# Performance work log

Hardware: AMD Instinct MI355X
Metric: run time of the kernel (lower is better)

Reference implementation:

```python
import jax, jax.numpy as jnp
import numpy as np

INPUT_DIM = 256
OUTPUT_DIM = 16
MAX_HIDDEN = 768
NUM_NODES = INPUT_DIM + OUTPUT_DIM + MAX_HIDDEN          # 1040
NUM_MIDDLE = OUTPUT_DIM + MAX_HIDDEN                     # 784
BATCH = 32768


def setup_inputs() -> dict:
    key = jax.random.key(0)
    k1, k2, k3, k4 = jax.random.split(key, 4)
    x = jax.random.normal(k1, (BATCH, INPUT_DIM), dtype=jnp.float32)
    weight = jax.random.normal(k2, (NUM_NODES, NUM_MIDDLE), dtype=jnp.float32) * 0.1
    bias = jax.random.normal(k3, (NUM_MIDDLE,), dtype=jnp.float32) * 0.1
    connectivity = jax.random.randint(k4, (NUM_NODES, NUM_MIDDLE), 0, 2, dtype=jnp.int32)
    node_existence = jnp.ones((NUM_MIDDLE,), dtype=jnp.int32)
    return {
        "x": x,
        "weight": weight,
        "bias": bias,
        "connectivity": connectivity,
        "node_existence": node_existence,
        "output_dim": OUTPUT_DIM,
    }


def reference(x, weight, bias, connectivity, node_existence, output_dim):
    B = x.shape[0]
    N, M = weight.shape                 # num_nodes, num_middle_result_nodes
    input_dim = N - M
    eff = weight * connectivity.astype(weight.dtype)   # [N, M] masked weights
    ex = node_existence.astype(weight.dtype)           # [M]
    results0 = jnp.zeros((B, N), dtype=x.dtype).at[:, :input_dim].set(x)
    node_idx = jnp.arange(N)

    def step(results, i):
        # only nodes < input_dim + i feed node i (faithful to growing slice)
        valid = (node_idx < input_dim + i).astype(eff.dtype)   # [N]
        w_col = jnp.take(eff, i, axis=1) * valid               # [N]
        res = results @ w_col                                   # [B]
        res = (jax.nn.sigmoid(res) + bias[i]) * ex[i]
        results = jax.lax.dynamic_update_slice(results, res[:, None], (0, input_dim + i))
        return results, None

    results, _ = jax.lax.scan(step, results0, jnp.arange(M))
    return results[:, -output_dim:]
```

## Files before the change

kernel.cpp:

```cpp
#include <hip/hip_runtime.h>
#include <cstdint>
#include <cstddef>

#define INPUT_DIM 256
#define OUT_DIM   16
#define NMID      784
#define NNODE     1040
#define MROW      768
#define KB        16
#define NBLK      49
#define NMCH      24
#define BATCH     32768
#define UNITW     520
#define XROW      264

typedef float f32x4 __attribute__((ext_vector_type(4)));
typedef __bf16 bf16x8 __attribute__((ext_vector_type(8)));

#define GLL16(gp, lp)                                                        \
  __builtin_amdgcn_global_load_lds(                                          \
      (const __attribute__((address_space(1))) unsigned int*)(gp),           \
      (__attribute__((address_space(3))) unsigned int*)(lp), 16, 0, 0)

static __device__ __forceinline__ unsigned int f2bf(float f) {
  unsigned int u = __builtin_bit_cast(unsigned int, f);
  u += 0x7fffu + ((u >> 16) & 1u);
  return u >> 16;
}
static __device__ __forceinline__ float bf2f(unsigned short h) {
  unsigned int u = ((unsigned int)h) << 16;
  return __builtin_bit_cast(float, u);
}
static __device__ __forceinline__ float bflo(unsigned int w) {
  return __builtin_bit_cast(float, w << 16);
}
static __device__ __forceinline__ float bfhi(unsigned int w) {
  return __builtin_bit_cast(float, w & 0xffff0000u);
}

__global__ __launch_bounds__(256) void prep_efft(
    const float* __restrict__ w, const int* __restrict__ conn,
    const int* __restrict__ ex, unsigned short* __restrict__ effX,
    unsigned short* __restrict__ effM) {
  __shared__ unsigned short tile[64][66];
  const int j0 = blockIdx.x * 64;
  const int i0 = blockIdx.y * 64;
  const int tx = threadIdx.x & 63;
  const int ty = threadIdx.x >> 6;
  const int i  = i0 + tx;
  for (int t = 0; t < 16; ++t) {
    int j = j0 + t * 4 + ty;
    float v = 0.f;
    if (j < NNODE && i < NMID && j < INPUT_DIM + i) {
      float e = (j >= INPUT_DIM) ? (float)ex[j - INPUT_DIM] : 1.f;
      v = w[(size_t)j * NMID + i] * (float)conn[(size_t)j * NMID + i] * e;
    }
    tile[t * 4 + ty][tx] = (unsigned short)f2bf(v);
  }
  __syncthreads();
  const int i_loc = threadIdx.x >> 2;
  const int jq    = threadIdx.x & 3;
  const int iw    = i0 + i_loc;
  const int jbase = j0 + jq * 16;
  if (iw < NMID) {
    if (jbase + 16 <= INPUT_DIM) {
      #pragma unroll
      for (int c = 0; c < 16; ++c)
        effX[(size_t)iw * INPUT_DIM + jbase + c] = tile[jq * 16 + c][i_loc];
    } else if (jbase >= INPUT_DIM && (jbase - INPUT_DIM + 16) <= MROW) {
      #pragma unroll
      for (int c = 0; c < 16; ++c)
        effM[(size_t)iw * MROW + (jbase - INPUT_DIM) + c] =
            tile[jq * 16 + c][i_loc];
    }
  }
}

__global__ __launch_bounds__(64) void prep_cvec(
    const unsigned short* __restrict__ effM, const float* __restrict__ w,
    const int* __restrict__ conn, const int* __restrict__ ex,
    const float* __restrict__ bias, float* __restrict__ cvec) {
  const int i = blockIdx.x;
  const int l = threadIdx.x;
  float s = 0.f;
  for (int jm = l; jm < MROW; jm += 64)
    s += bf2f(effM[(size_t)i * MROW + jm]) * bias[jm];
  {
    int jm = MROW + l;
    if (jm < NMID && jm < i) {
      size_t idx = (size_t)(INPUT_DIM + jm) * NMID + i;
      s += w[idx] * (float)conn[idx] * (float)ex[jm] * bias[jm];
    }
  }
  for (int off = 32; off; off >>= 1) s += __shfl_down(s, off, 64);
  if (l == 0) cvec[i] = s;
}

__global__ __launch_bounds__(256) void prep_wpack(
    const float* __restrict__ w, const int* __restrict__ conn,
    const int* __restrict__ ex, const float* __restrict__ cvec,
    unsigned short* __restrict__ wpk) {
  const int b = blockIdx.x;
  const int k = threadIdx.x >> 4;
  const int c = threadIdx.x & 15;
  const int src = KB * b + k;
  const int dst = KB * b + c;
  float v = 0.f;
  if (k < c) {
    size_t idx = (size_t)(INPUT_DIM + src) * NMID + dst;
    v = w[idx] * (float)conn[idx] * (float)ex[src];
  } else if (k == c) {
    v = cvec[src];
  }
  wpk[b * 256 + k * 16 + c] = (unsigned short)f2bf(v);
}

__global__ __launch_bounds__(256)
__attribute__((amdgpu_waves_per_eu(2, 4))) void pgemm(
    const float* __restrict__ x, const unsigned short* __restrict__ effX,
    unsigned short* __restrict__ Pt, int slab_off, int slabsz) {
  __shared__ __align__(16) unsigned short xs[64][XROW];

  const int tid = threadIdx.x;
  const int l   = tid & 63;
  const int wv  = tid >> 6;
  const int g   = l >> 4;
  const int r16 = l & 15;
  const int bb  = blockIdx.x * 64;

  {
    const int row = tid >> 2;
    const int q   = tid & 3;
    const float* xr = x + (size_t)(slab_off + bb + row) * INPUT_DIM + q * 64;
    unsigned short* xd = &xs[row][q * 64];
    #pragma unroll
    for (int i = 0; i < 16; ++i) {
      float4 v = *(const float4*)(xr + 4 * i);
      uint2 u;
      u.x = f2bf(v.x) | (f2bf(v.y) << 16);
      u.y = f2bf(v.z) | (f2bf(v.w) << 16);
      *(uint2*)(xd + 4 * i) = u;
    }
  }
  __syncthreads();

  for (int nb = wv; nb < NBLK; nb += 4) {
    const unsigned short* ap =
        effX + (size_t)(nb * 16 + r16) * INPUT_DIM + 8 * g;
    uint4 a[8];
    #pragma unroll
    for (int c = 0; c < 8; ++c) a[c] = *(const uint4*)(ap + 32 * c);

    #pragma unroll
    for (int s = 0; s < 4; ++s) {
      f32x4 acc = {0.f, 0.f, 0.f, 0.f};
      #pragma unroll
      for (int c = 0; c < 8; ++c) {
        uint4 braw = *(const uint4*)&xs[s * 16 + r16][32 * c + 8 * g];
        acc = __builtin_amdgcn_mfma_f32_16x16x32_bf16(
            __builtin_bit_cast(bf16x8, a[c]), __builtin_bit_cast(bf16x8, braw),
            acc, 0, 0, 0);
      }
      #pragma unroll
      for (int i = 0; i < 4; ++i)
        Pt[(size_t)(nb * 16 + 4 * g + i) * slabsz + bb + s * 16 + r16] =
            (unsigned short)f2bf(acc[i]);
    }
  }
}

__global__ __launch_bounds__(256)
__attribute__((amdgpu_waves_per_eu(2, 2))) void net_main(
    const unsigned short* __restrict__ Pt,
    const unsigned short* __restrict__ effM,
    const unsigned short* __restrict__ wpk,
    const float* __restrict__ bias, const int* __restrict__ ex,
    float* __restrict__ out, int slab_off, int slabsz) {
  __shared__ __align__(16) unsigned short Bs[2][3][8][UNITW];
  __shared__ __align__(16) unsigned short wtriL[2][256];
  __shared__ float scrS[4][320];

  const int tid = threadIdx.x;
  const int l   = tid & 63;
  const int wv  = tid >> 6;
  const int g   = l >> 4;
  const int r16 = l & 15;
  const int rb  = (blockIdx.x * 4 + wv) * 16;
  float* myscr = scrS[wv];

  uint4 sfrag[NMCH];
  #pragma unroll
  for (int c = 0; c < NMCH; ++c) {
    uint4 z; z.x = z.y = z.z = z.w = 0u;
    sfrag[c] = z;
  }

#define STAGE_B(nb, t)                                                        \
  {                                                                           \
    _Pragma("unroll")                                                         \
    for (int q_ = 0; q_ < 2; ++q_) {                                          \
      const int rp_ = wv + 4 * q_;                             \
      const int r_  = 2 * rp_ + (l >> 5);                    \
      const int cl_ = (l & 31) ^ (r_ & 7);                                    \
      const unsigned short* gs_ =                                             \
          effM + (size_t)(16 * (t) + r_) * MROW + cl_ * 8;                    \
      GLL16(gs_, &Bs[nb][0][rp_][0]);                                         \
      if ((t) >= 17) GLL16(gs_ + 256, &Bs[nb][1][rp_][0]);                    \
      if ((t) >= 33) GLL16(gs_ + 512, &Bs[nb][2][rp_][0]);                    \
    }                                                                         \
  }

  if (wv == 0) {
    uint2 t0 = *(const uint2*)(wpk + l * 4);
    *(uint2*)&wtriL[0][l * 4] = t0;
  }
  __syncthreads();

  for (int b = 0; b < NBLK; ++b) {
    const int cur = b & 1;

    if (b + 1 < NBLK) {
      STAGE_B(cur ^ 1, b + 1);
      if (wv == 0) {
        uint2 tw = *(const uint2*)(wpk + (b + 1) * 256 + l * 4);
        *(uint2*)&wtriL[cur ^ 1][l * 4] = tw;
      }
    }

    uint2 praw = *(const uint2*)(Pt + (size_t)(KB * b + r16) * slabsz +
                                 rb + 4 * g);

    f32x4 ac0 = {0.f, 0.f, 0.f, 0.f}, ac1 = ac0, ac2 = ac0, ac3 = ac0;
#define CHUNK(c)                                                              \
  {                                                                           \
    const int pp_ = (c) >> 3, cc_ = (c) & 7;                                  \
    uint4 braw = *(const uint4*)&Bs[cur][pp_][r16 >> 1]                       \
        [(r16 & 1) * 256 + (((cc_ * 4 + g) ^ (r16 & 7)) * 8)];                \
    f32x4& a_ = ((c) & 3) == 0 ? ac0 : ((c) & 3) == 1 ? ac1                   \
               : ((c) & 3) == 2 ? ac2 : ac3;                                  \
    a_ = __builtin_amdgcn_mfma_f32_16x16x32_bf16(                             \
        __builtin_bit_cast(bf16x8, sfrag[(c)]),                               \
        __builtin_bit_cast(bf16x8, braw), a_, 0, 0, 0);                       \
  }
    if (b >= 1) {
      CHUNK(0) CHUNK(1) CHUNK(2) CHUNK(3)
      CHUNK(4) CHUNK(5) CHUNK(6) CHUNK(7)
    }
    if (b >= 17) {
      CHUNK(8) CHUNK(9) CHUNK(10) CHUNK(11)
      CHUNK(12) CHUNK(13) CHUNK(14) CHUNK(15)
    }
    if (b >= 33) {
      CHUNK(16) CHUNK(17) CHUNK(18) CHUNK(19)
      CHUNK(20) CHUNK(21) CHUNK(22) CHUNK(23)
    }
#undef CHUNK
    f32x4 accsum = (ac0 + ac1) + (ac2 + ac3);
    accsum[0] += bflo(praw.x);
    accsum[1] += bfhi(praw.x);
    accsum[2] += bflo(praw.y);
    accsum[3] += bfhi(praw.y);

    #pragma unroll
    for (int i = 0; i < 4; ++i)
      myscr[(4 * g + i) * 20 + r16] = accsum[i];
    float acc_t[16];
    #pragma unroll
    for (int c = 0; c < 16; ++c)
      acc_t[c] = myscr[r16 * 20 + c];

    const unsigned short* wt = wtriL[cur];
    #pragma unroll
    for (int k = 0; k < 16; ++k) {
      const uint4 w0 = *(const uint4*)&wt[k * 16];
      const uint4 w1 = *(const uint4*)&wt[k * 16 + 8];
      const unsigned int wd[8] = {w0.x, w0.y, w0.z, w0.w,
                                  w1.x, w1.y, w1.z, w1.w};
      float xk = acc_t[k] + ((k & 1) ? bfhi(wd[k >> 1]) : bflo(wd[k >> 1]));
      float s  = __builtin_amdgcn_rcpf(
          1.f + __builtin_amdgcn_exp2f(xk * -1.44269504088896341f));
      acc_t[k] = s;
      #pragma unroll
      for (int c = k + 1; c < 16; ++c) {
        float wc = (c & 1) ? bfhi(wd[c >> 1]) : bflo(wd[c >> 1]);
        acc_t[c] = __builtin_fmaf(s, wc, acc_t[c]);
      }
    }

    if (b == NBLK - 1) {
      const size_t orow = (size_t)(slab_off + rb + r16) * OUT_DIM;
      #pragma unroll
      for (int i = 0; i < 4; ++i) {
        int oc = 4 * g + i;
        int mi = NMID - OUT_DIM + oc;
        out[orow + oc] = (acc_t[oc] + bias[mi]) * (float)ex[mi];
      }
    } else {
      const int cml = (b >> 1) & 7;
      const int vb = 8 * (g & 1);
      uint4 packed;
      packed.x = f2bf(acc_t[vb + 0]) | (f2bf(acc_t[vb + 1]) << 16);
      packed.y = f2bf(acc_t[vb + 2]) | (f2bf(acc_t[vb + 3]) << 16);
      packed.z = f2bf(acc_t[vb + 4]) | (f2bf(acc_t[vb + 5]) << 16);
      packed.w = f2bf(acc_t[vb + 6]) | (f2bf(acc_t[vb + 7]) << 16);
      const bool part = ((g >> 1) == (b & 1));
#define PACKW(base)                                                           \
  {                                                                           \
    _Pragma("unroll")                                                         \
    for (int c2 = 0; c2 < 8; ++c2)                                            \
      if (c2 == cml) {                                                        \
        if (part) sfrag[(base) + c2] = packed;                                \
      }                                                                       \
  }
      if (b < 16) {
        PACKW(0)
      } else if (b < 32) {
        PACKW(8)
      } else {
        PACKW(16)
      }
#undef PACKW
    }

    __syncthreads();
  }
#undef STAGE_B
}

extern "C" void kernel_launch(void* const* d_in, const int* in_sizes, int n_in,
                              void* d_out, int out_size, void* d_ws, size_t ws_size,
                              hipStream_t stream) {
  const float* x      = (const float*)d_in[0];
  const float* weight = (const float*)d_in[1];
  const float* bias   = (const float*)d_in[2];
  const int*   conn   = (const int*)d_in[3];
  const int*   ex     = (const int*)d_in[4];

  char* ws = (char*)d_ws;
  size_t off = 0;
  unsigned short* effX = (unsigned short*)(ws + off); off += (size_t)NMID * INPUT_DIM * 2;
  unsigned short* effM = (unsigned short*)(ws + off); off += (size_t)NMID * MROW * 2;
  float*          cvec = (float*)(ws + off);          off += (size_t)NMID * 4;
  unsigned short* wpk  = (unsigned short*)(ws + off); off += (size_t)NBLK * 256 * 2;
  off = (off + 255) & ~(size_t)255;
  const size_t fixed = off;

  int nslabs = 1;
  while (nslabs < 16 &&
         fixed + (size_t)NMID * (BATCH / nslabs) * 2 > ws_size)
    nslabs <<= 1;
  const int slabsz = BATCH / nslabs;
  unsigned short* Pt = (unsigned short*)(ws + fixed);

  prep_efft<<<dim3(16, 13), 256, 0, stream>>>(weight, conn, ex, effX, effM);
  prep_cvec<<<dim3(NMID), 64, 0, stream>>>(effM, weight, conn, ex, bias, cvec);
  prep_wpack<<<dim3(NBLK), 256, 0, stream>>>(weight, conn, ex, cvec, wpk);

  for (int s = 0; s < nslabs; ++s) {
    pgemm<<<dim3(slabsz / 64), 256, 0, stream>>>(
        x, effX, Pt, s * slabsz, slabsz);
    net_main<<<dim3(slabsz / 64), 256, 0, stream>>>(
        Pt, effM, wpk, bias, ex, (float*)d_out, s * slabsz, slabsz);
  }
}
```

Baseline: 239.7 us.

## Tile Pt layout, swap MFMA operands, use bpermute transpose and fp32 triangle weights

Stores the projected input Pt in a 16x16 tiled layout, so each pgemm wave writes 8-byte chunks and each net_main lane reads a contiguous tile per block instead of strided rows. The MFMA operand order is swapped so the accumulator comes out transposed, and the LDS scratch round-trip that transposed the 16x16 tile is replaced by ds_bpermute lane exchanges. The triangular intra-block weights are kept in fp32 in LDS, which removes bf16 unpacking in the serial sigmoid chain and improves precision. Removing the scratch array and relaxing waves_per_eu to 3-4 aims for higher occupancy, at the risk of register pressure from the 24 sfrag registers.

```diff
diff --git a/kernel.cpp b/kernel.cpp
--- a/kernel.cpp
+++ b/kernel.cpp
@@ -99,7 +99,7 @@
 __global__ __launch_bounds__(256) void prep_wpack(
     const float* __restrict__ w, const int* __restrict__ conn,
     const int* __restrict__ ex, const float* __restrict__ cvec,
-    unsigned short* __restrict__ wpk) {
+    float* __restrict__ wpk) {
   const int b = blockIdx.x;
   const int k = threadIdx.x >> 4;
   const int c = threadIdx.x & 15;
@@ -112,7 +112,7 @@
   } else if (k == c) {
     v = cvec[src];
   }
-  wpk[b * 256 + k * 16 + c] = (unsigned short)f2bf(v);
+  wpk[b * 256 + k * 16 + c] = v;
 }
 
 __global__ __launch_bounds__(256)
@@ -161,24 +161,24 @@
             __builtin_bit_cast(bf16x8, a[c]), __builtin_bit_cast(bf16x8, braw),
             acc, 0, 0, 0);
       }
-      #pragma unroll
-      for (int i = 0; i < 4; ++i)
-        Pt[(size_t)(nb * 16 + 4 * g + i) * slabsz + bb + s * 16 + r16] =
-            (unsigned short)f2bf(acc[i]);
+      uint2 u;
+      u.x = f2bf(acc[0]) | (f2bf(acc[1]) << 16);
+      u.y = f2bf(acc[2]) | (f2bf(acc[3]) << 16);
+      *(uint2*)&Pt[((size_t)(((bb >> 4) + s) * NBLK + nb) << 8) +
+                   r16 * 16 + 4 * g] = u;
     }
   }
 }
 
 __global__ __launch_bounds__(256)
-__attribute__((amdgpu_waves_per_eu(2, 2))) void net_main(
+__attribute__((amdgpu_waves_per_eu(3, 4))) void net_main(
     const unsigned short* __restrict__ Pt,
     const unsigned short* __restrict__ effM,
-    const unsigned short* __restrict__ wpk,
+    const float* __restrict__ wpk,
     const float* __restrict__ bias, const int* __restrict__ ex,
     float* __restrict__ out, int slab_off, int slabsz) {
   __shared__ __align__(16) unsigned short Bs[2][3][8][UNITW];
-  __shared__ __align__(16) unsigned short wtriL[2][256];
-  __shared__ float scrS[4][320];
+  __shared__ __align__(16) float wtriF[2][256];
 
   const int tid = threadIdx.x;
   const int l   = tid & 63;
@@ -186,7 +186,8 @@
   const int g   = l >> 4;
   const int r16 = l & 15;
   const int rb  = (blockIdx.x * 4 + wv) * 16;
-  float* myscr = scrS[wv];
+  const int idx16 = (l ^ 16) << 2;
+  const int idx32 = (l ^ 32) << 2;
 
   uint4 sfrag[NMCH];
   #pragma unroll
@@ -210,10 +211,8 @@
     }                                                                         \
   }
 
-  if (wv == 0) {
-    uint2 t0 = *(const uint2*)(wpk + l * 4);
-    *(uint2*)&wtriL[0][l * 4] = t0;
-  }
+  if (wv == 0)
+    *(float4*)&wtriF[0][l * 4] = *(const float4*)(wpk + l * 4);
   __syncthreads();
 
   for (int b = 0; b < NBLK; ++b) {
@@ -221,14 +220,13 @@
 
     if (b + 1 < NBLK) {
       STAGE_B(cur ^ 1, b + 1);
-      if (wv == 0) {
-        uint2 tw = *(const uint2*)(wpk + (b + 1) * 256 + l * 4);
-        *(uint2*)&wtriL[cur ^ 1][l * 4] = tw;
-      }
-    }
-
-    uint2 praw = *(const uint2*)(Pt + (size_t)(KB * b + r16) * slabsz +
-                                 rb + 4 * g);
+      if (wv == 0)
+        *(float4*)&wtriF[cur ^ 1][l * 4] =
+            *(const float4*)(wpk + (b + 1) * 256 + l * 4);
+    }
+
+    uint2 praw = *(const uint2*)&Pt[((size_t)((rb >> 4) * NBLK + b) << 8) +
+                                    r16 * 16 + 4 * g];
 
     f32x4 ac0 = {0.f, 0.f, 0.f, 0.f}, ac1 = ac0, ac2 = ac0, ac3 = ac0;
 #define CHUNK(c)                                                              \
@@ -239,8 +237,8 @@
     f32x4& a_ = ((c) & 3) == 0 ? ac0 : ((c) & 3) == 1 ? ac1                   \
                : ((c) & 3) == 2 ? ac2 : ac3;                                  \
     a_ = __builtin_amdgcn_mfma_f32_16x16x32_bf16(                             \
-        __builtin_bit_cast(bf16x8, sfrag[(c)]),                               \
-        __builtin_bit_cast(bf16x8, braw), a_, 0, 0, 0);                       \
+        __builtin_bit_cast(bf16x8, braw),                                     \
+        __builtin_bit_cast(bf16x8, sfrag[(c)]), a_, 0, 0, 0);                 \
   }
     if (b >= 1) {
       CHUNK(0) CHUNK(1) CHUNK(2) CHUNK(3)
@@ -256,54 +254,81 @@
     }
 #undef CHUNK
     f32x4 accsum = (ac0 + ac1) + (ac2 + ac3);
-    accsum[0] += bflo(praw.x);
-    accsum[1] += bfhi(praw.x);
-    accsum[2] += bflo(praw.y);
-    accsum[3] += bfhi(praw.y);
-
-    #pragma unroll
-    for (int i = 0; i < 4; ++i)
-      myscr[(4 * g + i) * 20 + r16] = accsum[i];
+    float v0 = accsum[0] + bflo(praw.x);
+    float v1 = accsum[1] + bfhi(praw.x);
+    float v2 = accsum[2] + bflo(praw.y);
+    float v3 = accsum[3] + bfhi(praw.y);
+
+    float q0 = __builtin_bit_cast(float,
+        __builtin_amdgcn_ds_bpermute(idx16, __builtin_bit_cast(int, v0)));
+    float q1 = __builtin_bit_cast(float,
+        __builtin_amdgcn_ds_bpermute(idx16, __builtin_bit_cast(int, v1)));
+    float q2 = __builtin_bit_cast(float,
+        __builtin_amdgcn_ds_bpermute(idx16, __builtin_bit_cast(int, v2)));
+    float q3 = __builtin_bit_cast(float,
+        __builtin_amdgcn_ds_bpermute(idx16, __builtin_bit_cast(int, v3)));
+    const bool glo = (g & 1) == 0;
+    float p8[8];
+    p8[0] = glo ? v0 : q0;
+    p8[1] = glo ? v1 : q1;
+    p8[2] = glo ? v2 : q2;
+    p8[3] = glo ? v3 : q3;
+    p8[4] = glo ? q0 : v0;
+    p8[5] = glo ? q1 : v1;
+    p8[6] = glo ? q2 : v2;
+    p8[7] = glo ? q3 : v3;
+    const bool plo = g < 2;
     float acc_t[16];
     #pragma unroll
-    for (int c = 0; c < 16; ++c)
-      acc_t[c] = myscr[r16 * 20 + c];
-
-    const unsigned short* wt = wtriL[cur];
+    for (int j = 0; j < 8; ++j) {
+      float rj = __builtin_bit_cast(float,
+          __builtin_amdgcn_ds_bpermute(idx32, __builtin_bit_cast(int, p8[j])));
+      acc_t[j]     = plo ? p8[j] : rj;
+      acc_t[8 + j] = plo ? rj : p8[j];
+    }
+
+    const float* wt = &wtriF[cur][0];
     #pragma unroll
     for (int k = 0; k < 16; ++k) {
-      const uint4 w0 = *(const uint4*)&wt[k * 16];
-      const uint4 w1 = *(const uint4*)&wt[k * 16 + 8];
-      const unsigned int wd[8] = {w0.x, w0.y, w0.z, w0.w,
-                                  w1.x, w1.y, w1.z, w1.w};
-      float xk = acc_t[k] + ((k & 1) ? bfhi(wd[k >> 1]) : bflo(wd[k >> 1]));
+      float wr[16];
+      #pragma unroll
+      for (int q = k >> 2; q < 4; ++q) {
+        float4 wq = *(const float4*)(wt + k * 16 + q * 4);
+        wr[q * 4 + 0] = wq.x; wr[q * 4 + 1] = wq.y;
+        wr[q * 4 + 2] = wq.z; wr[q * 4 + 3] = wq.w;
+      }
+      float xk = acc_t[k] + wr[k];
       float s  = __builtin_amdgcn_rcpf(
           1.f + __builtin_amdgcn_exp2f(xk * -1.44269504088896341f));
       acc_t[k] = s;
       #pragma unroll
-      for (int c = k + 1; c < 16; ++c) {
-        float wc = (c & 1) ? bfhi(wd[c >> 1]) : bflo(wd[c >> 1]);
-        acc_t[c] = __builtin_fmaf(s, wc, acc_t[c]);
-      }
+      for (int c = k + 1; c < 16; ++c)
+        acc_t[c] = __builtin_fmaf(s, wr[c], acc_t[c]);
     }
 
     if (b == NBLK - 1) {
       const size_t orow = (size_t)(slab_off + rb + r16) * OUT_DIM;
       #pragma unroll
       for (int i = 0; i < 4; ++i) {
+        float a01 = (g & 1) ? acc_t[4 + i] : acc_t[i];
+        float a23 = (g & 1) ? acc_t[12 + i] : acc_t[8 + i];
+        float ov  = (g & 2) ? a23 : a01;
         int oc = 4 * g + i;
         int mi = NMID - OUT_DIM + oc;
-        out[orow + oc] = (acc_t[oc] + bias[mi]) * (float)ex[mi];
+        out[orow + oc] = (ov + bias[mi]) * (float)ex[mi];
       }
     } else {
+      float pv[8];
+      #pragma unroll
+      for (int j = 0; j < 8; ++j)
+        pv[j] = (g & 1) ? acc_t[8 + j] : acc_t[j];
+      uint4 packed;
+      packed.x = f2bf(pv[0]) | (f2bf(pv[1]) << 16);
+      packed.y = f2bf(pv[2]) | (f2bf(pv[3]) << 16);
+      packed.z = f2bf(pv[4]) | (f2bf(pv[5]) << 16);
+      packed.w = f2bf(pv[6]) | (f2bf(pv[7]) << 16);
+      const bool part = ((g >> 1) == (b & 1));
       const int cml = (b >> 1) & 7;
-      const int vb = 8 * (g & 1);
-      uint4 packed;
-      packed.x = f2bf(acc_t[vb + 0]) | (f2bf(acc_t[vb + 1]) << 16);
-      packed.y = f2bf(acc_t[vb + 2]) | (f2bf(acc_t[vb + 3]) << 16);
-      packed.z = f2bf(acc_t[vb + 4]) | (f2bf(acc_t[vb + 5]) << 16);
-      packed.w = f2bf(acc_t[vb + 6]) | (f2bf(acc_t[vb + 7]) << 16);
-      const bool part = ((g >> 1) == (b & 1));
 #define PACKW(base)                                                           \
   {                                                                           \
     _Pragma("unroll")                                                         \
@@ -341,13 +366,13 @@
   unsigned short* effX = (unsigned short*)(ws + off); off += (size_t)NMID * INPUT_DIM * 2;
   unsigned short* effM = (unsigned short*)(ws + off); off += (size_t)NMID * MROW * 2;
   float*          cvec = (float*)(ws + off);          off += (size_t)NMID * 4;
-  unsigned short* wpk  = (unsigned short*)(ws + off); off += (size_t)NBLK * 256 * 2;
+  float*          wpk  = (float*)(ws + off);          off += (size_t)NBLK * 256 * 4;
   off = (off + 255) & ~(size_t)255;
   const size_t fixed = off;
 
   int nslabs = 1;
   while (nslabs < 16 &&
-         fixed + (size_t)NMID * (BATCH / nslabs) * 2 > ws_size)
+         fixed + (size_t)(BATCH / nslabs) * NBLK * 16 * 2 > ws_size)
     nslabs <<= 1;
   const int slabsz = BATCH / nslabs;
   unsigned short* Pt = (unsigned short*)(ws + fixed);
```

After: 601.0 us. 2.51x slower.

## Software-pipeline block solve with next block's MFMA accumulation

Applied to the files above, without the earlier changes.

Restructures the sequential block loop so iteration b runs the MFMA accumulation for block b with the older sfrag state while the triangular sigmoid solve for block b-1 happens in the same iteration. The contribution of the just-solved block is then added with one extra MFMA using only the new fragment. The goal is to take the long MFMA chain off the critical dependency path of the serial solve so the two can overlap. It needs a third wtri buffer, a prologue and an epilogue, and adds one MFMA per block.

```diff
diff --git a/kernel.cpp b/kernel.cpp
--- a/kernel.cpp
+++ b/kernel.cpp
@@ -36,6 +36,26 @@
 }
 static __device__ __forceinline__ float bfhi(unsigned int w) {
   return __builtin_bit_cast(float, w & 0xffff0000u);
+}
+
+static __device__ __forceinline__ void solve16(float* acc_t,
+                                               const unsigned short* wt) {
+  #pragma unroll
+  for (int k = 0; k < 16; ++k) {
+    const uint4 w0 = *(const uint4*)&wt[k * 16];
+    const uint4 w1 = *(const uint4*)&wt[k * 16 + 8];
+    const unsigned int wd[8] = {w0.x, w0.y, w0.z, w0.w,
+                                w1.x, w1.y, w1.z, w1.w};
+    float xk = acc_t[k] + ((k & 1) ? bfhi(wd[k >> 1]) : bflo(wd[k >> 1]));
+    float s  = __builtin_amdgcn_rcpf(
+        1.f + __builtin_amdgcn_exp2f(xk * -1.44269504088896341f));
+    acc_t[k] = s;
+    #pragma unroll
+    for (int c = k + 1; c < 16; ++c) {
+      float wc = (c & 1) ? bfhi(wd[c >> 1]) : bflo(wd[c >> 1]);
+      acc_t[c] = __builtin_fmaf(s, wc, acc_t[c]);
+    }
+  }
 }
 
 __global__ __launch_bounds__(256) void prep_efft(
@@ -177,7 +197,7 @@
     const float* __restrict__ bias, const int* __restrict__ ex,
     float* __restrict__ out, int slab_off, int slabsz) {
   __shared__ __align__(16) unsigned short Bs[2][3][8][UNITW];
-  __shared__ __align__(16) unsigned short wtriL[2][256];
+  __shared__ __align__(16) unsigned short wtriL[3][256];
   __shared__ float scrS[4][320];
 
   const int tid = threadIdx.x;
@@ -209,22 +229,30 @@
       if ((t) >= 33) GLL16(gs_ + 512, &Bs[nb][2][rp_][0]);                    \
     }                                                                         \
   }
-
-  if (wv == 0) {
-    uint2 t0 = *(const uint2*)(wpk + l * 4);
-    *(uint2*)&wtriL[0][l * 4] = t0;
+#define STAGE_W(t)                                                            \
+  if (wv == 0)                                                                \
+    *(uint2*)&wtriL[(t) % 3][l * 4] = *(const uint2*)(wpk + (t) * 256 + l * 4);
+
+  STAGE_W(0);
+  STAGE_B(1, 1);
+  STAGE_W(1);
+  {
+    uint2 praw = *(const uint2*)(Pt + (size_t)r16 * slabsz + rb + 4 * g);
+    myscr[(4 * g + 0) * 20 + r16] = bflo(praw.x);
+    myscr[(4 * g + 1) * 20 + r16] = bfhi(praw.x);
+    myscr[(4 * g + 2) * 20 + r16] = bflo(praw.y);
+    myscr[(4 * g + 3) * 20 + r16] = bfhi(praw.y);
   }
   __syncthreads();
 
-  for (int b = 0; b < NBLK; ++b) {
+  for (int b = 1; b < NBLK; ++b) {
     const int cur = b & 1;
+    const int pb  = b - 1;
+    const int cstar = pb >> 1;
 
     if (b + 1 < NBLK) {
       STAGE_B(cur ^ 1, b + 1);
-      if (wv == 0) {
-        uint2 tw = *(const uint2*)(wpk + (b + 1) * 256 + l * 4);
-        *(uint2*)&wtriL[cur ^ 1][l * 4] = tw;
-      }
+      STAGE_W(b + 1);
     }
 
     uint2 praw = *(const uint2*)(Pt + (size_t)(KB * b + r16) * slabsz +
@@ -242,7 +270,7 @@
         __builtin_bit_cast(bf16x8, sfrag[(c)]),                               \
         __builtin_bit_cast(bf16x8, braw), a_, 0, 0, 0);                       \
   }
-    if (b >= 1) {
+    {
       CHUNK(0) CHUNK(1) CHUNK(2) CHUNK(3)
       CHUNK(4) CHUNK(5) CHUNK(6) CHUNK(7)
     }
@@ -255,55 +283,21 @@
       CHUNK(20) CHUNK(21) CHUNK(22) CHUNK(23)
     }
 #undef CHUNK
-    f32x4 accsum = (ac0 + ac1) + (ac2 + ac3);
-    accsum[0] += bflo(praw.x);
-    accsum[1] += bfhi(praw.x);
-    accsum[2] += bflo(praw.y);
-    accsum[3] += bfhi(praw.y);
-
-    #pragma unroll
-    for (int i = 0; i < 4; ++i)
-      myscr[(4 * g + i) * 20 + r16] = accsum[i];
+
     float acc_t[16];
     #pragma unroll
     for (int c = 0; c < 16; ++c)
       acc_t[c] = myscr[r16 * 20 + c];
-
-    const unsigned short* wt = wtriL[cur];
-    #pragma unroll
-    for (int k = 0; k < 16; ++k) {
-      const uint4 w0 = *(const uint4*)&wt[k * 16];
-      const uint4 w1 = *(const uint4*)&wt[k * 16 + 8];
-      const unsigned int wd[8] = {w0.x, w0.y, w0.z, w0.w,
-                                  w1.x, w1.y, w1.z, w1.w};
-      float xk = acc_t[k] + ((k & 1) ? bfhi(wd[k >> 1]) : bflo(wd[k >> 1]));
-      float s  = __builtin_amdgcn_rcpf(
-          1.f + __builtin_amdgcn_exp2f(xk * -1.44269504088896341f));
-      acc_t[k] = s;
-      #pragma unroll
-      for (int c = k + 1; c < 16; ++c) {
-        float wc = (c & 1) ? bfhi(wd[c >> 1]) : bflo(wd[c >> 1]);
-        acc_t[c] = __builtin_fmaf(s, wc, acc_t[c]);
-      }
-    }
-
-    if (b == NBLK - 1) {
-      const size_t orow = (size_t)(slab_off + rb + r16) * OUT_DIM;
-      #pragma unroll
-      for (int i = 0; i < 4; ++i) {
-        int oc = 4 * g + i;
-        int mi = NMID - OUT_DIM + oc;
-        out[orow + oc] = (acc_t[oc] + bias[mi]) * (float)ex[mi];
-      }
-    } else {
-      const int cml = (b >> 1) & 7;
-      const int vb = 8 * (g & 1);
-      uint4 packed;
-      packed.x = f2bf(acc_t[vb + 0]) | (f2bf(acc_t[vb + 1]) << 16);
-      packed.y = f2bf(acc_t[vb + 2]) | (f2bf(acc_t[vb + 3]) << 16);
-      packed.z = f2bf(acc_t[vb + 4]) | (f2bf(acc_t[vb + 5]) << 16);
-      packed.w = f2bf(acc_t[vb + 6]) | (f2bf(acc_t[vb + 7]) << 16);
-      const bool part = ((g >> 1) == (b & 1));
+    solve16(acc_t, wtriL[pb % 3]);
+
+    const int cml = cstar & 7;
+    const int vb  = 8 * (g & 1);
+    uint4 packed;
+    packed.x = f2bf(acc_t[vb + 0]) | (f2bf(acc_t[vb + 1]) << 16);
+    packed.y = f2bf(acc_t[vb + 2]) | (f2bf(acc_t[vb + 3]) << 16);
+    packed.z = f2bf(acc_t[vb + 4]) | (f2bf(acc_t[vb + 5]) << 16);
+    packed.w = f2bf(acc_t[vb + 6]) | (f2bf(acc_t[vb + 7]) << 16);
+    const bool part = ((g >> 1) == (pb & 1));
 #define PACKW(base)                                                           \
   {                                                                           \
     _Pragma("unroll")                                                         \
@@ -312,19 +306,62 @@
         if (part) sfrag[(base) + c2] = packed;                                \
       }                                                                       \
   }
-      if (b < 16) {
-        PACKW(0)
-      } else if (b < 32) {
-        PACKW(8)
-      } else {
-        PACKW(16)
-      }
+    if (pb < 16) {
+      PACKW(0)
+    } else if (pb < 32) {
+      PACKW(8)
+    } else {
+      PACKW(16)
+    }
 #undef PACKW
-    }
+
+    {
+      uint4 onlynew;
+      onlynew.x = part ? packed.x : 0u;
+      onlynew.y = part ? packed.y : 0u;
+      onlynew.z = part ? packed.z : 0u;
+      onlynew.w = part ? packed.w : 0u;
+      const int slot = ((cml * 4 + g) ^ (r16 & 7)) * 8;
+      uint4 braw;
+      if (cstar < 8)
+        braw = *(const uint4*)&Bs[cur][0][r16 >> 1][(r16 & 1) * 256 + slot];
+      else if (cstar < 16)
+        braw = *(const uint4*)&Bs[cur][1][r16 >> 1][(r16 & 1) * 256 + slot];
+      else
+        braw = *(const uint4*)&Bs[cur][2][r16 >> 1][(r16 & 1) * 256 + slot];
+      ac0 = __builtin_amdgcn_mfma_f32_16x16x32_bf16(
+          __builtin_bit_cast(bf16x8, onlynew), __builtin_bit_cast(bf16x8, braw),
+          ac0, 0, 0, 0);
+    }
+
+    f32x4 accsum = (ac0 + ac1) + (ac2 + ac3);
+    accsum[0] += bflo(praw.x);
+    accsum[1] += bfhi(praw.x);
+    accsum[2] += bflo(praw.y);
+    accsum[3] += bfhi(praw.y);
+    #pragma unroll
+    for (int i = 0; i < 4; ++i)
+      myscr[(4 * g + i) * 20 + r16] = accsum[i];
 
     __syncthreads();
   }
+#undef STAGE_W
 #undef STAGE_B
+
+  {
+    float acc_t[16];
+    #pragma unroll
+    for (int c = 0; c < 16; ++c)
+      acc_t[c] = myscr[r16 * 20 + c];
+    solve16(acc_t, wtriL[(NBLK - 1) % 3]);
+    const size_t orow = (size_t)(slab_off + rb + r16) * OUT_DIM;
+    #pragma unroll
+    for (int i = 0; i < 4; ++i) {
+      int oc = 4 * g + i;
+      int mi = NMID - OUT_DIM + oc;
+      out[orow + oc] = (acc_t[oc] + bias[mi]) * (float)ex[mi];
+    }
+  }
 }
 
 extern "C" void kernel_launch(void* const* d_in, const int* in_sizes, int n_in,
```

After: 229.0 us. -4.4%, faster.
